# Performance work log

Measured on AMD Instinct MI355X. Metric: run time of the kernel, lower is better.

The kernel has to match this reference:

```python
import jax, jax.numpy as jnp
import numpy as np
from jax import lax

EPS = 1e-5
C, H, W, G = 512, 32, 32, 32


def instance_norm(x):
    # torch InstanceNorm2d: affine=False, biased variance over (H,W)
    mu = x.mean(axis=(2, 3), keepdims=True)
    var = ((x - mu) ** 2).mean(axis=(2, 3), keepdims=True)
    return (x - mu) / jnp.sqrt(var + EPS)


def conv2d(x, w, stride=1, padding=0, groups=1, lhs_dilation=None):
    return lax.conv_general_dilated(
        x, w, (stride, stride), [(padding, padding)] * 2,
        lhs_dilation=lhs_dilation, feature_group_count=groups,
        dimension_numbers=('NCHW', 'OIHW', 'NCHW'))


def leaky_relu(x):
    return jnp.where(x >= 0, x, 0.2 * x)


def unfold(img, k, s):
    # img: (C,H,W) -> (nH*nW, C, k, k); matches torch unfold(1,k,s).unfold(2,k,s)
    c, h, w = img.shape
    nH = (h - k) // s + 1
    nW = (w - k) // s + 1
    rows = []
    for i in range(k):
        cols = [img[:, i:i + s * (nH - 1) + 1:s, j:j + s * (nW - 1) + 1:s] for j in range(k)]
        rows.append(jnp.stack(cols, axis=-1))  # (C,nH,nW,k)
    p = jnp.stack(rows, axis=-2)  # (C,nH,nW,k,k)
    return p.transpose(1, 2, 0, 3, 4).reshape(nH * nW, c, k, k)


def ral(bg, fg, rate=2, ksize=3, scale=10.0):
    # Region Affinity Layer (contextual-attention style), batch = 1
    b, c, h, w = fg.shape
    fh, fw = h // rate, w // rate
    # bilinear downsample by exactly 2 (half-pixel) == 2x2 average pooling
    fg_small = fg.reshape(b, c, fh, rate, fw, rate).mean(axis=(3, 5))
    bk = 2 * rate
    bg_patches = unfold(jnp.pad(bg, ((0, 0), (0, 0), (1, 1), (1, 1)))[0], bk, rate)      # (256,C,4,4)
    fg_patches = unfold(jnp.pad(fg_small, ((0, 0), (0, 0), (1, 1), (1, 1)))[0], ksize, 1)  # (256,C,3,3)
    norm = jnp.sqrt((fg_patches ** 2).sum(axis=(1, 2, 3), keepdims=True))
    fgp_n = fg_patches / jnp.maximum(norm, 1e-4)
    score = conv2d(fg_small, fgp_n, padding=1)        # (1,256,16,16)
    attn = jax.nn.softmax(score * scale, axis=1)
    # conv_transpose2d(attn, bg_patches, stride=rate, padding=1) via lhs dilation
    w_t = jnp.flip(bg_patches, axis=(-2, -1)).transpose(1, 0, 2, 3)  # (C,256,4,4)
    return conv2d(attn, w_t, padding=bk - 2, lhs_dilation=(rate, rate)) / 4.0  # (1,C,32,32)


def forward(x, gus, w_sk3, b_sk3, w_sk5, b_sk5, w_sk7, b_sk7,
            w_fc, b_fc, w_fc0, b_fc0, w_fc1, b_fc1, w_fc2, b_fc2, w_down, w_fuse):
    # ---- SKConv (M=3 branches: k=3/5/7, groups=32) ----
    feas = []
    for wgt, bias, pad in ((w_sk3, b_sk3, 1), (w_sk5, b_sk5, 2), (w_sk7, b_sk7, 3)):
        f = conv2d(x, wgt, padding=pad, groups=G) + bias[None, :, None, None]
        feas.append(jax.nn.relu(instance_norm(f)))
    feas = jnp.stack(feas, axis=1)                # (B,3,C,H,W)
    fea_s = feas.sum(axis=1).mean(axis=(2, 3))    # (B,C) global pool
    fea_z = fea_s @ w_fc.T + b_fc                 # (B,32)
    att = jnp.stack([fea_z @ w_fc0.T + b_fc0,
                     fea_z @ w_fc1.T + b_fc1,
                     fea_z @ w_fc2.T + b_fc2], axis=1)  # (B,3,C)
    att = jax.nn.softmax(att, axis=1)[..., None, None]
    out_32 = (feas * att).sum(axis=1)             # (1,C,32,32)
    out_res = out_32
    out_32 = ral(out_32, out_32)
    b, c, h, w = out_32.shape
    # ---- gaussian-weighted broadcast sum: (P,H,W)x(C,H,W)->(P,C)->raw reshape ----
    gus_out = jnp.einsum('pxy,cxy->pc', gus, out_32[0]).reshape(b, c, h, w)
    # ---- CSA patch correlation ----
    csa2_in = jax.nn.sigmoid(out_32)
    p_fff = unfold(jnp.pad(out_32, ((0, 0), (0, 0), (1, 1), (1, 1)))[0], 3, 1)    # (1024,C,3,3)
    p_f = unfold(jnp.pad(csa2_in, ((0, 0), (0, 0), (1, 1), (1, 1)))[0], 3, 1)     # (1024,C,3,3)
    p_conv = unfold(csa2_in[0], 1, 1)                                             # (1024,C,1,1)
    csa_a = (p_conv * p_f).mean(axis=1)                                           # (1024,3,3)
    csa_a = jax.nn.softmax(csa_a.reshape(h * w, 9), axis=1).reshape(h * w, 1, 3, 3)
    out_csa = (csa_a * p_fff).sum(axis=(-2, -1)).reshape(b, c, h, w)
    # ---- fuse ----
    z = jnp.concatenate([gus_out, out_csa], axis=1)       # (1,1024,32,32)
    z = leaky_relu(instance_norm(conv2d(z, w_down)))
    z = jnp.concatenate([z, out_res], axis=1)             # (1,1024,32,32)
    return leaky_relu(instance_norm(conv2d(z, w_fuse)))   # (1,512,32,32)


def _gaussian_buffer():
    # util.gussin(1.5): gaussian centered at every grid position of a 32x32 map
    v = 1.5
    r = np.arange(32)
    i, k, x, y = np.meshgrid(r, r, r, r, indexing='ij')
    g = np.exp(-((x - i) ** 2 + (y - k) ** 2) / (2 * v * v)) / (2 * np.pi * v * v)
    return jnp.asarray(g.reshape(32 * 32, 32, 32), dtype=jnp.float32)


def setup_inputs():
    key = jax.random.key(0)
    ks = jax.random.split(key, 12)
    s = 0.02
    return {
        'x': jax.random.normal(ks[0], (1, C, H, W), jnp.float32),
        'gus': _gaussian_buffer(),
        'w_sk3': jax.random.normal(ks[1], (C, C // G, 3, 3), jnp.float32) * s,
        'b_sk3': jnp.zeros((C,), jnp.float32),
        'w_sk5': jax.random.normal(ks[2], (C, C // G, 5, 5), jnp.float32) * s,
        'b_sk5': jnp.zeros((C,), jnp.float32),
        'w_sk7': jax.random.normal(ks[3], (C, C // G, 7, 7), jnp.float32) * s,
        'b_sk7': jnp.zeros((C,), jnp.float32),
        'w_fc': jax.random.normal(ks[4], (32, C), jnp.float32) * s,
        'b_fc': jnp.zeros((32,), jnp.float32),
        'w_fc0': jax.random.normal(ks[5], (C, 32), jnp.float32) * s,
        'b_fc0': jnp.zeros((C,), jnp.float32),
        'w_fc1': jax.random.normal(ks[6], (C, 32), jnp.float32) * s,
        'b_fc1': jnp.zeros((C,), jnp.float32),
        'w_fc2': jax.random.normal(ks[7], (C, 32), jnp.float32) * s,
        'b_fc2': jnp.zeros((C,), jnp.float32),
        'w_down': jax.random.normal(ks[8], (512, 1024, 1, 1), jnp.float32) * s,
        'w_fuse': jax.random.normal(ks[9], (512, 1024, 1, 1), jnp.float32) * s,
    }


def reference(x, gus, w_sk3, b_sk3, w_sk5, b_sk5, w_sk7, b_sk7, w_fc, b_fc,
              w_fc0, b_fc0, w_fc1, b_fc1, w_fc2, b_fc2, w_down, w_fuse):
    return forward(x, gus, w_sk3, b_sk3, w_sk5, b_sk5, w_sk7, b_sk7,
                   w_fc, b_fc, w_fc0, b_fc0, w_fc1, b_fc1, w_fc2, b_fc2,
                   w_down, w_fuse)
```

## Files before the change

kernel.cpp:

```cpp
#include <hip/hip_runtime.h>
#include <math.h>

#define EPSN 1e-5f

typedef __attribute__((ext_vector_type(8))) short bf16x8;
typedef __attribute__((ext_vector_type(4))) float f32x4;

__device__ __forceinline__ ushort f2bf(float f) {
  unsigned u = __float_as_uint(f);
  unsigned r = (u + 0x7fff + ((u >> 16) & 1)) >> 16;
  return (ushort)r;
}
__device__ __forceinline__ float bf2f(ushort h) {
  return __uint_as_float(((unsigned)h) << 16);
}

__device__ __forceinline__ void breduce2(float& a, float& b, float* lds) {
#pragma unroll
  for (int o = 32; o > 0; o >>= 1) {
    a += __shfl_down(a, o);
    b += __shfl_down(b, o);
  }
  int lane = threadIdx.x & 63, wid = threadIdx.x >> 6;
  __syncthreads();
  if (lane == 0) { lds[wid] = a; lds[4 + wid] = b; }
  __syncthreads();
  a = lds[0] + lds[1] + lds[2] + lds[3];
  b = lds[4] + lds[5] + lds[6] + lds[7];
}

__device__ __forceinline__ float breduce_sum(float v, float* lds) {
#pragma unroll
  for (int o = 32; o > 0; o >>= 1) v += __shfl_down(v, o);
  int lane = threadIdx.x & 63, wid = threadIdx.x >> 6;
  __syncthreads();
  if (lane == 0) lds[wid] = v;
  __syncthreads();
  return lds[0] + lds[1] + lds[2] + lds[3];
}

__device__ __forceinline__ float breduce_max(float v, float* lds) {
#pragma unroll
  for (int o = 32; o > 0; o >>= 1) v = fmaxf(v, __shfl_down(v, o));
  int lane = threadIdx.x & 63, wid = threadIdx.x >> 6;
  __syncthreads();
  if (lane == 0) lds[wid] = v;
  __syncthreads();
  return fmaxf(fmaxf(lds[0], lds[1]), fmaxf(lds[2], lds[3]));
}

__global__ void pre_kernel(const float* __restrict__ gus,
                           const float* __restrict__ wdown,
                           const float* __restrict__ wfuse,
                           const float* __restrict__ w3,
                           const float* __restrict__ w5,
                           const float* __restrict__ w7,
                           ushort* __restrict__ gus_bf,
                           ushort* __restrict__ wdown_bf,
                           ushort* __restrict__ wfuse_bf,
                           ushort* __restrict__ resd,
                           ushort* __restrict__ Apk_g,
                           ushort* __restrict__ Acomb) {
  int bid = blockIdx.x, tid = threadIdx.x;
  if (bid < 2048) {
    int i = bid * 1024 + tid * 4;
    if (i < 1048576) {
      float4 v = *(const float4*)&gus[i];
      int m = i >> 10, n = i & 1023;
      int y = n >> 5, x = n & 31;
      int idxb = ((y >> 1) << 4) + (x >> 1);
      int py = y & 1;
      ushort2 e0 = {f2bf(v.x), f2bf(v.z)};
      ushort2 e1 = {f2bf(v.y), f2bf(v.w)};
      *(ushort2*)&gus_bf[(size_t)m * 1024 + (py * 2 + 0) * 256 + idxb] = e0;
      *(ushort2*)&gus_bf[(size_t)m * 1024 + (py * 2 + 1) * 256 + idxb] = e1;
    } else {
      const float* src; ushort* dst; int off;
      if (i < 1572864) { src = wdown; dst = wdown_bf; off = i - 1048576; }
      else { src = wfuse; dst = wfuse_bf; off = i - 1572864; }
      float4 v = *(const float4*)&src[off];
      ushort4 o = {f2bf(v.x), f2bf(v.y), f2bf(v.z), f2bf(v.w)};
      *(ushort4*)&dst[off] = o;
    }
  } else if (bid < 2304) {
    int t8 = (bid - 2048) * 256 + tid;
    uint4 z = {0u, 0u, 0u, 0u};
#pragma unroll
    for (int k = 0; k < 4; ++k) *(uint4*)&resd[(size_t)(t8 + k * 65536) * 8] = z;
  } else if (bid < 5056) {
    int i2 = (bid - 2304) * 256 + tid;
    int g = i2 / 22016;
    int r = i2 - g * 22016;
    int p = r >> 9;
    int r5 = r & 511;
    int quad = r5 >> 7, m16 = (r5 >> 3) & 15, j = r & 7;
    int k = quad * 8 + j, tp = k >> 4, ic = k & 15;
    float val = 0.f;
    if (p < 25) {
      int t = 2 * p + tp;
      if (t < 49) val = w7[(size_t)(g * 16 + m16) * 784 + ic * 49 + t];
    } else if (p < 38) {
      int t = 2 * (p - 25) + tp;
      if (t < 25) val = w5[(size_t)(g * 16 + m16) * 400 + ic * 25 + t];
    } else {
      int t = 2 * (p - 38) + tp;
      if (t < 9) val = w3[(size_t)(g * 16 + m16) * 144 + ic * 9 + t];
    }
    Apk_g[i2] = f2bf(val);
  } else {
    int j = (bid - 5056) * 256 + tid;
    uint4 z = {0u, 0u, 0u, 0u};
    ((uint4*)Acomb)[j] = z;
  }
}

__global__ __launch_bounds__(256) void sk_mfma(const float* __restrict__ x,
                                               const ushort* __restrict__ Apk_g,
                                               ushort* __restrict__ feasRawH) {
  __shared__ ushort xg[10 * 38 * 24];
  int bid = blockIdx.x, tid = threadIdx.x;
  int g = bid >> 3, sl = bid & 7, y0 = sl * 4;
  for (int i = tid; i < 4560; i += 256) ((uint*)xg)[i] = 0u;
  __syncthreads();
  for (int i = tid; i < 5120; i += 256) {
    int lr = i >> 9, ic = (i >> 5) & 15, xc = i & 31;
    int y = y0 + lr - 3;
    if ((unsigned)y < 32u)
      xg[(lr * 38 + xc + 3) * 24 + ic] =
          f2bf(x[(size_t)(g * 16 + ic) * 1024 + y * 32 + xc]);
  }
  __syncthreads();
  int wv = tid >> 6, lane = tid & 63, quad = lane >> 4, m16 = lane & 15;
  int qh = (quad & 1) * 8, tp = quad >> 1;
  const ushort* Ag = Apk_g + (size_t)g * 22016;
  f32x4 acc[2][3] = {};
  for (int p = 0; p < 25; ++p) {
    bf16x8 af = *(const bf16x8*)&Ag[(p * 4 + quad) * 128 + m16 * 8];
    int t = 2 * p + tp;
    if (t > 48) t = 48;
    int ky = t / 7, kx = t - ky * 7;
#pragma unroll
    for (int ti = 0; ti < 2; ++ti) {
      int T = wv + ti * 4, tl = T >> 1, x0c = (T & 1) * 16;
      bf16x8 bf = *(const bf16x8*)&xg[((tl + ky) * 38 + x0c + m16 + kx) * 24 + qh];
      acc[ti][2] = __builtin_amdgcn_mfma_f32_16x16x32_bf16(af, bf, acc[ti][2], 0, 0, 0);
    }
  }
  for (int p = 0; p < 13; ++p) {
    bf16x8 af = *(const bf16x8*)&Ag[((p + 25) * 4 + quad) * 128 + m16 * 8];
    int t = 2 * p + tp;
    if (t > 24) t = 24;
    int ky = t / 5, kx = t - ky * 5;
#pragma unroll
    for (int ti = 0; ti < 2; ++ti) {
      int T = wv + ti * 4, tl = T >> 1, x0c = (T & 1) * 16;
      bf16x8 bf =
          *(const bf16x8*)&xg[((tl + ky + 1) * 38 + x0c + m16 + kx + 1) * 24 + qh];
      acc[ti][1] = __builtin_amdgcn_mfma_f32_16x16x32_bf16(af, bf, acc[ti][1], 0, 0, 0);
    }
  }
  for (int p = 0; p < 5; ++p) {
    bf16x8 af = *(const bf16x8*)&Ag[((p + 38) * 4 + quad) * 128 + m16 * 8];
    int t = 2 * p + tp;
    if (t > 8) t = 8;
    int ky = t / 3, kx = t - ky * 3;
#pragma unroll
    for (int ti = 0; ti < 2; ++ti) {
      int T = wv + ti * 4, tl = T >> 1, x0c = (T & 1) * 16;
      bf16x8 bf =
          *(const bf16x8*)&xg[((tl + ky + 2) * 38 + x0c + m16 + kx + 2) * 24 + qh];
      acc[ti][0] = __builtin_amdgcn_mfma_f32_16x16x32_bf16(af, bf, acc[ti][0], 0, 0, 0);
    }
  }
  int cb = g * 16 + quad * 4;
#pragma unroll
  for (int ti = 0; ti < 2; ++ti) {
    int T = wv + ti * 4, tl = T >> 1, x0c = (T & 1) * 16;
    int pos = (y0 + tl) * 32 + x0c + m16;
#pragma unroll
    for (int br = 0; br < 3; ++br)
#pragma unroll
      for (int r = 0; r < 4; ++r)
        feasRawH[(size_t)(br * 512 + cb + r) * 1024 + pos] = f2bf(acc[ti][br][r]);
  }
}

__global__ __launch_bounds__(256) void sk_norm(const ushort* __restrict__ rawH,
                                               ushort* __restrict__ feasH,
                                               float* __restrict__ bmean) {
  __shared__ float red[8];
  int mc = blockIdx.x, tid = threadIdx.x;
  float v[4];
  {
    ushort4 h = *(const ushort4*)&rawH[(size_t)mc * 1024 + tid * 4];
    v[0] = bf2f(h.x); v[1] = bf2f(h.y); v[2] = bf2f(h.z); v[3] = bf2f(h.w);
  }
  float s = 0.f, ss = 0.f;
#pragma unroll
  for (int r = 0; r < 4; ++r) { s += v[r]; ss += v[r] * v[r]; }
  breduce2(s, ss, red);
  float mean = s * (1.f / 1024.f);
  float var = ss * (1.f / 1024.f) - mean * mean;
  float inv = rsqrtf(var + EPSN);
  float rs = 0.f;
  ushort4 o;
#pragma unroll
  for (int r = 0; r < 4; ++r) {
    float t = (v[r] - mean) * inv;
    t = t > 0.f ? t : 0.f;
    ((ushort*)&o)[r] = f2bf(t);
    rs += t;
  }
  *(ushort4*)&feasH[(size_t)mc * 1024 + tid * 4] = o;
  float tot = breduce_sum(rs, red);
  if (tid == 0) bmean[mc] = tot * (1.f / 1024.f);
}

__global__ __launch_bounds__(256) void blend_fc(
    const ushort* __restrict__ feasH, const float* __restrict__ bmean,
    const float* __restrict__ wfc, const float* __restrict__ bfc,
    const float* __restrict__ w0, const float* __restrict__ b0,
    const float* __restrict__ w1, const float* __restrict__ b1,
    const float* __restrict__ w2, const float* __restrict__ b2,
    float* __restrict__ res, ushort* __restrict__ Zt2,
    ushort* __restrict__ resd) {
  __shared__ float sfea[512];
  __shared__ float zpart[8][32];
  __shared__ float zz[32];
  __shared__ float lv[3][32];
  __shared__ float attb[3][32];
  __shared__ float tile[32][33];
  int tid = threadIdx.x;
  int pb = blockIdx.x * 32, cb = blockIdx.y * 32;
  for (int c = tid; c < 512; c += 256)
    sfea[c] = bmean[c] + bmean[512 + c] + bmean[1024 + c];
  __syncthreads();
  {
    int j = tid & 31, seg = tid >> 5;
    float p = 0.f;
    for (int c = seg * 64; c < seg * 64 + 64; ++c) p += sfea[c] * wfc[j * 512 + c];
    zpart[seg][j] = p;
  }
  __syncthreads();
  if (tid < 32) {
    float d = bfc[tid];
#pragma unroll
    for (int s = 0; s < 8; ++s) d += zpart[s][tid];
    zz[tid] = d;
  }
  __syncthreads();
  if (tid < 96) {
    int m = tid >> 5, cl = tid & 31;
    const float* wm = (m == 0) ? w0 : (m == 1) ? w1 : w2;
    const float* bm = (m == 0) ? b0 : (m == 1) ? b1 : b2;
    float l = bm[cb + cl];
#pragma unroll
    for (int j = 0; j < 32; ++j) l += zz[j] * wm[(cb + cl) * 32 + j];
    lv[m][cl] = l;
  }
  __syncthreads();
  if (tid < 32) {
    float l0 = lv[0][tid], l1 = lv[1][tid], l2 = lv[2][tid];
    float mx = fmaxf(l0, fmaxf(l1, l2));
    float e0 = expf(l0 - mx), e1 = expf(l1 - mx), e2 = expf(l2 - mx);
    float inv = 1.f / (e0 + e1 + e2);
    attb[0][tid] = e0 * inv; attb[1][tid] = e1 * inv; attb[2][tid] = e2 * inv;
  }
  __syncthreads();
  int tx = tid & 31, ty = tid >> 5;
  int pos = pb + tx;
  int yy = pos >> 5, xx = pos & 31;
  int ki0 = (yy + 1) & 1, pi0 = (yy + 1 - ki0) >> 1;
  int kj0 = (xx + 1) & 1, pj0 = (xx + 1 - kj0) >> 1;
#pragma unroll
  for (int r = 0; r < 4; ++r) {
    int cl = ty + r * 8;
    int c = cb + cl;
    float v = bf2f(feasH[(size_t)c * 1024 + pos]) * attb[0][cl] +
              bf2f(feasH[(size_t)(512 + c) * 1024 + pos]) * attb[1][cl] +
              bf2f(feasH[(size_t)(1024 + c) * 1024 + pos]) * attb[2][cl];
    res[c * 1024 + pos] = v;
    tile[cl][tx] = v;
    ushort bv16 = f2bf(v);
#pragma unroll
    for (int ai = 0; ai < 2; ++ai) {
      int ki = ki0 + 2 * ai, pi = pi0 - ai;
      if ((unsigned)pi >= 16u) continue;
#pragma unroll
      for (int aj = 0; aj < 2; ++aj) {
        int kj = kj0 + 2 * aj, pj = pj0 - aj;
        if ((unsigned)pj >= 16u) continue;
        resd[((size_t)(ki * 4 + kj) << 17) + (size_t)c * 256 + pi * 16 + pj] = bv16;
      }
    }
  }
  __syncthreads();
#pragma unroll
  for (int r = 0; r < 4; ++r) {
    int pl = ty + r * 8;
    Zt2[(size_t)(pb + pl) * 1024 + 512 + cb + tx] = f2bf(tile[tx][pl]);
  }
}

__global__ __launch_bounds__(256) void gram_part2(const float* __restrict__ res,
                                                  float* __restrict__ Apart) {
  __shared__ float ch[4][324];
  int tid = threadIdx.x;
  int qb = blockIdx.x * 64, pb = blockIdx.y * 64;
  int kc = blockIdx.z;
  int tx = tid & 15, ty = tid >> 4;
  for (int i = tid; i < 4 * 324; i += 256) ((float*)ch)[i] = 0.f;
  int pi = (pb + ty * 4) >> 4, pj = (pb + ty * 4) & 15;
  int qi = (qb + tx * 4) >> 4, qj = (qb + tx * 4) & 15;
  int lane = tid & 63, wv = tid >> 6;
  int sr = lane >> 2, sc = (lane & 3) * 4;
  float acc[4][4] = {};
  for (int c0 = kc * 16; c0 < kc * 16 + 16; c0 += 4) {
    __syncthreads();
    {
      const float* src = res + (size_t)(c0 + wv) * 1024 + (2 * sr) * 32 + 2 * sc;
      float4 r0a = *(const float4*)src;
      float4 r0b = *(const float4*)(src + 4);
      float4 r1a = *(const float4*)(src + 32);
      float4 r1b = *(const float4*)(src + 36);
      float* dst = &ch[wv][(sr + 1) * 18 + sc + 1];
      dst[0] = 0.25f * (r0a.x + r0a.y + r1a.x + r1a.y);
      dst[1] = 0.25f * (r0a.z + r0a.w + r1a.z + r1a.w);
      dst[2] = 0.25f * (r0b.x + r0b.y + r1b.x + r1b.y);
      dst[3] = 0.25f * (r0b.z + r0b.w + r1b.z + r1b.w);
    }
    __syncthreads();
#pragma unroll
    for (int cc = 0; cc < 4; ++cc) {
      float ps[3][6], qs[3][6];
#pragma unroll
      for (int u = 0; u < 3; ++u) {
        const float* pr = &ch[cc][(pi + u) * 18 + pj];
        const float* qr = &ch[cc][(qi + u) * 18 + qj];
#pragma unroll
        for (int t = 0; t < 6; ++t) { ps[u][t] = pr[t]; qs[u][t] = qr[t]; }
      }
#pragma unroll
      for (int u = 0; u < 3; ++u)
#pragma unroll
        for (int v = 0; v < 3; ++v)
#pragma unroll
          for (int i = 0; i < 4; ++i)
#pragma unroll
            for (int j = 0; j < 4; ++j)
              acc[i][j] += ps[u][v + i] * qs[u][v + j];
    }
  }
#pragma unroll
  for (int i = 0; i < 4; ++i) {
    float4 o4 = {acc[i][0], acc[i][1], acc[i][2], acc[i][3]};
    *(float4*)&Apart[(size_t)kc * 65536 + (pb + ty * 4 + i) * 256 + qb + tx * 4] = o4;
  }
}

__global__ __launch_bounds__(256) void attn_soft4(const float* __restrict__ Apart,
                                                  ushort* __restrict__ Acomb) {
  __shared__ float red[8];
  int q = blockIdx.x, t = threadIdx.x;
  float d = 0.f, s = 0.f;
#pragma unroll
  for (int k = 0; k < 32; ++k) {
    d += Apart[(size_t)k * 65536 + t * 257];
    s += Apart[(size_t)k * 65536 + q * 256 + t];
  }
  float invn = 10.f / fmaxf(sqrtf(fmaxf(d, 0.f)), 1e-4f);
  float v = s * invn;
  float mx = breduce_max(v, red);
  float e = expf(v - mx);
  float sm = breduce_sum(e, red);
  ushort val = f2bf(e / sm);
  int qi = q >> 4, qj = q & 15;
#pragma unroll
  for (int ki = 0; ki < 4; ++ki) {
    int y = 2 * qi + ki - 1;
    if ((unsigned)y >= 32u) continue;
#pragma unroll
    for (int kj = 0; kj < 4; ++kj) {
      int x = 2 * qj + kj - 1;
      if ((unsigned)x >= 32u) continue;
      int cls = (y & 1) * 2 + (x & 1);
      int idx = ((y >> 1) << 4) + (x >> 1);
      int seg = ((ki >> 1) << 1) + (kj >> 1);
      Acomb[(size_t)(cls * 256 + idx) * 1024 + seg * 256 + t] = val;
    }
  }
}

__global__ __launch_bounds__(256) void tconv2(const ushort* __restrict__ Acomb,
                                              const ushort* __restrict__ resd,
                                              float* __restrict__ orlt,
                                              float* __restrict__ sigt,
                                              ushort* __restrict__ orlT) {
  __shared__ float tl[64][33];
  int tid = threadIdx.x;
  int wv = tid >> 6, lane = tid & 63, quad = lane >> 4, m16 = lane & 15;
  int nb = blockIdx.x * 32;
  int mb = blockIdx.y * 64;
  int cls = blockIdx.y >> 2;
  int py = cls >> 1, px = cls & 1;
  int row0 = mb + wv * 16 + m16;
  const ushort* Ap = Acomb + (size_t)row0 * 1024 + quad * 8;
  f32x4 ac0 = {0.f, 0.f, 0.f, 0.f}, ac1 = ac0;
#pragma unroll
  for (int sg = 0; sg < 4; ++sg) {
    int ki = 2 * (sg >> 1) + 1 - py;
    int kj = 2 * (sg & 1) + 1 - px;
    const ushort* Bp =
        resd + ((size_t)(ki * 4 + kj) << 17) + (size_t)(nb + m16) * 256 + quad * 8;
    const ushort* As = Ap + sg * 256;
#pragma unroll 2
    for (int k0 = 0; k0 < 256; k0 += 32) {
      bf16x8 af = *(const bf16x8*)(As + k0);
      bf16x8 b0 = *(const bf16x8*)(Bp + k0);
      bf16x8 b1 = *(const bf16x8*)(Bp + 16 * 256 + k0);
      ac0 = __builtin_amdgcn_mfma_f32_16x16x32_bf16(af, b0, ac0, 0, 0, 0);
      ac1 = __builtin_amdgcn_mfma_f32_16x16x32_bf16(af, b1, ac1, 0, 0, 0);
    }
  }
  int rloc0 = wv * 16 + quad * 4;
  f32x4 accs[2] = {ac0, ac1};
#pragma unroll
  for (int nt = 0; nt < 2; ++nt) {
    int c = nb + nt * 16 + m16;
#pragma unroll
    for (int r = 0; r < 4; ++r) {
      int rl = rloc0 + r;
      int idx = (mb + rl) & 255;
      int y = ((idx >> 4) << 1) + py;
      int x = ((idx & 15) << 1) + px;
      int n = y * 32 + x;
      float v = accs[nt][r] * 0.25f;
      orlt[n * 512 + c] = v;
      sigt[n * 512 + c] = 1.f / (1.f + expf(-v));
      tl[rl][nt * 16 + m16] = v;
    }
  }
  __syncthreads();
  int r_l = tid & 63;
#pragma unroll
  for (int k = 0; k < 8; ++k) {
    int c_l = (tid >> 6) + k * 4;
    orlT[(size_t)(nb + c_l) * 1024 + mb + r_l] = f2bf(tl[r_l][c_l]);
  }
}

__global__ __launch_bounds__(256) void gus_csa(
    const ushort* __restrict__ gus_bf, const ushort* __restrict__ orlT,
    const float* __restrict__ sigt, const float* __restrict__ orlt,
    ushort* __restrict__ Zt) {
  __shared__ float red9[4][9];
  __shared__ float a9s[9];
  int tid = threadIdx.x;
  if (blockIdx.x < 128) {
    const int K = 1024;
    int wv = tid >> 6, lane = tid & 63;
    int quad = lane >> 4, m16 = lane & 15;
    int nb = (blockIdx.x & 7) * 64, mb = (blockIdx.x >> 3) * 64;
    const ushort* Ap = gus_bf + (size_t)(mb + wv * 16 + m16) * K + quad * 8;
    const ushort* Bp = orlT + (size_t)(nb + m16) * K + quad * 8;
    f32x4 ac0 = {0.f, 0.f, 0.f, 0.f}, ac1 = ac0, ac2 = ac0, ac3 = ac0;
#pragma unroll 2
    for (int k0 = 0; k0 < K; k0 += 32) {
      bf16x8 af = *(const bf16x8*)(Ap + k0);
      bf16x8 b0 = *(const bf16x8*)(Bp + k0);
      bf16x8 b1 = *(const bf16x8*)(Bp + (size_t)16 * K + k0);
      bf16x8 b2 = *(const bf16x8*)(Bp + (size_t)32 * K + k0);
      bf16x8 b3 = *(const bf16x8*)(Bp + (size_t)48 * K + k0);
      ac0 = __builtin_amdgcn_mfma_f32_16x16x32_bf16(af, b0, ac0, 0, 0, 0);
      ac1 = __builtin_amdgcn_mfma_f32_16x16x32_bf16(af, b1, ac1, 0, 0, 0);
      ac2 = __builtin_amdgcn_mfma_f32_16x16x32_bf16(af, b2, ac2, 0, 0, 0);
      ac3 = __builtin_amdgcn_mfma_f32_16x16x32_bf16(af, b3, ac3, 0, 0, 0);
    }
    int row = mb + wv * 16 + quad * 4;
    f32x4 accs[4] = {ac0, ac1, ac2, ac3};
#pragma unroll
    for (int nt = 0; nt < 4; ++nt) {
      int c = nb + nt * 16 + m16;
#pragma unroll
      for (int r = 0; r < 4; ++r) {
        int p = row + r;
        int pos = ((p & 1) << 9) + c;
        int kk = p >> 1;
        Zt[(size_t)pos * 1024 + kk] = f2bf(accs[nt][r]);
      }
    }
    return;
  }
  int n = blockIdx.x - 128;
  int ny = n >> 5, nx = n & 31;
  int c2 = tid * 2;
  int lane = tid & 63, wid = tid >> 6;
  float2 ctr = *(const float2*)&sigt[n * 512 + c2];
  float part[9];
#pragma unroll
  for (int u = 0; u < 3; ++u) {
    int yy = ny + u - 1;
#pragma unroll
    for (int v = 0; v < 3; ++v) {
      int xx = nx + v - 1;
      float2 nb2 = {0.f, 0.f};
      if ((unsigned)yy < 32u && (unsigned)xx < 32u)
        nb2 = *(const float2*)&sigt[(yy * 32 + xx) * 512 + c2];
      part[u * 3 + v] = ctr.x * nb2.x + ctr.y * nb2.y;
    }
  }
#pragma unroll
  for (int t = 0; t < 9; ++t)
#pragma unroll
    for (int o = 32; o > 0; o >>= 1) part[t] += __shfl_down(part[t], o);
  if (lane == 0)
#pragma unroll
    for (int t = 0; t < 9; ++t) red9[wid][t] = part[t];
  __syncthreads();
  if (tid == 0) {
    float a[9];
#pragma unroll
    for (int t = 0; t < 9; ++t)
      a[t] = (red9[0][t] + red9[1][t] + red9[2][t] + red9[3][t]) * (1.f / 512.f);
    float mx = a[0];
#pragma unroll
    for (int t = 1; t < 9; ++t) mx = fmaxf(mx, a[t]);
    float sum = 0.f;
#pragma unroll
    for (int t = 0; t < 9; ++t) { a[t] = expf(a[t] - mx); sum += a[t]; }
    float inv = 1.f / sum;
#pragma unroll
    for (int t = 0; t < 9; ++t) a9s[t] = a[t] * inv;
  }
  __syncthreads();
  float2 acc = {0.f, 0.f};
#pragma unroll
  for (int u = 0; u < 3; ++u) {
    int yy = ny + u - 1;
#pragma unroll
    for (int v = 0; v < 3; ++v) {
      int xx = nx + v - 1;
      if ((unsigned)yy < 32u && (unsigned)xx < 32u) {
        float w = a9s[u * 3 + v];
        float2 ov = *(const float2*)&orlt[(yy * 32 + xx) * 512 + c2];
        acc.x += w * ov.x;
        acc.y += w * ov.y;
      }
    }
  }
  int kk = 512 + (n >> 1);
  int pos0 = ((n & 1) << 9) + c2;
  Zt[(size_t)pos0 * 1024 + kk] = f2bf(acc.x);
  Zt[(size_t)(pos0 + 1) * 1024 + kk] = f2bf(acc.y);
}

__global__ __launch_bounds__(256) void mfma_gemm_ks(const ushort* __restrict__ A,
                                                    const ushort* __restrict__ Bt,
                                                    float* __restrict__ Cp,
                                                    int N) {
  const int KF = 1024;
  int tid = threadIdx.x;
  int wv = tid >> 6, lane = tid & 63;
  int quad = lane >> 4, m16 = lane & 15;
  int nb = blockIdx.x * 64, mb = blockIdx.y * 64;
  int kh = blockIdx.z;
  const ushort* Ap = A + (size_t)(mb + wv * 16 + m16) * KF + kh * 512 + quad * 8;
  const ushort* Bp = Bt + (size_t)(nb + m16) * KF + kh * 512 + quad * 8;
  f32x4 ac0 = {0.f, 0.f, 0.f, 0.f}, ac1 = ac0, ac2 = ac0, ac3 = ac0;
#pragma unroll 2
  for (int k0 = 0; k0 < 512; k0 += 32) {
    bf16x8 af = *(const bf16x8*)(Ap + k0);
    bf16x8 b0 = *(const bf16x8*)(Bp + k0);
    bf16x8 b1 = *(const bf16x8*)(Bp + (size_t)16 * KF + k0);
    bf16x8 b2 = *(const bf16x8*)(Bp + (size_t)32 * KF + k0);
    bf16x8 b3 = *(const bf16x8*)(Bp + (size_t)48 * KF + k0);
    ac0 = __builtin_amdgcn_mfma_f32_16x16x32_bf16(af, b0, ac0, 0, 0, 0);
    ac1 = __builtin_amdgcn_mfma_f32_16x16x32_bf16(af, b1, ac1, 0, 0, 0);
    ac2 = __builtin_amdgcn_mfma_f32_16x16x32_bf16(af, b2, ac2, 0, 0, 0);
    ac3 = __builtin_amdgcn_mfma_f32_16x16x32_bf16(af, b3, ac3, 0, 0, 0);
  }
  int row = mb + wv * 16 + quad * 4;
  float* C = Cp + (size_t)kh * 524288;
  f32x4 accs[4] = {ac0, ac1, ac2, ac3};
#pragma unroll
  for (int nt = 0; nt < 4; ++nt)
#pragma unroll
    for (int r = 0; r < 4; ++r)
      C[(size_t)(row + r) * N + nb + nt * 16 + m16] = accs[nt][r];
}

__global__ __launch_bounds__(256) void norm_down2(const float* __restrict__ ra,
                                                  ushort* __restrict__ Zt2) {
  __shared__ float red[8];
  int c = blockIdx.x, tid = threadIdx.x;
  float v[4];
  float s = 0.f, ss = 0.f;
#pragma unroll
  for (int r = 0; r < 4; ++r) {
    int i = c * 1024 + tid + r * 256;
    v[r] = ra[i] + ra[524288 + i];
    s += v[r];
    ss += v[r] * v[r];
  }
  breduce2(s, ss, red);
  float mean = s * (1.f / 1024.f);
  float var = ss * (1.f / 1024.f) - mean * mean;
  float inv = rsqrtf(var + EPSN);
#pragma unroll
  for (int r = 0; r < 4; ++r) {
    float t = (v[r] - mean) * inv;
    t = t >= 0.f ? t : 0.2f * t;
    Zt2[(size_t)(tid + r * 256) * 1024 + c] = f2bf(t);
  }
}

__global__ __launch_bounds__(256) void norm_leaky2(const float* __restrict__ ra,
                                                   float* __restrict__ out) {
  __shared__ float red[8];
  int c = blockIdx.x, tid = threadIdx.x;
  float v[4];
  float s = 0.f, ss = 0.f;
#pragma unroll
  for (int r = 0; r < 4; ++r) {
    int i = c * 1024 + tid + r * 256;
    v[r] = ra[i] + ra[524288 + i];
    s += v[r];
    ss += v[r] * v[r];
  }
  breduce2(s, ss, red);
  float mean = s * (1.f / 1024.f);
  float var = ss * (1.f / 1024.f) - mean * mean;
  float inv = rsqrtf(var + EPSN);
#pragma unroll
  for (int r = 0; r < 4; ++r) {
    float t = (v[r] - mean) * inv;
    out[c * 1024 + tid + r * 256] = t >= 0.f ? t : 0.2f * t;
  }
}

extern "C" void kernel_launch(void* const* d_in, const int* in_sizes, int n_in,
                              void* d_out, int out_size, void* d_ws, size_t ws_size,
                              hipStream_t stream) {
  const float* x = (const float*)d_in[0];
  const float* gus = (const float*)d_in[1];
  const float* w3 = (const float*)d_in[2];
  const float* w5 = (const float*)d_in[4];
  const float* w7 = (const float*)d_in[6];
  const float* wfc = (const float*)d_in[8];
  const float* bfc = (const float*)d_in[9];
  const float* w0 = (const float*)d_in[10];
  const float* b0 = (const float*)d_in[11];
  const float* w1 = (const float*)d_in[12];
  const float* b1 = (const float*)d_in[13];
  const float* w2 = (const float*)d_in[14];
  const float* b2 = (const float*)d_in[15];
  const float* wdown = (const float*)d_in[16];
  const float* wfuse = (const float*)d_in[17];

  float* ws = (float*)d_ws;
  ushort* feasH = (ushort*)ws;
  float* rawP = ws + 786432;
  ushort* Acomb = (ushort*)rawP;
  float* bmean = ws + 1835008;
  float* res = bmean + 1536;
  float* Zt2f = res + 524288;
  ushort* Zt2 = (ushort*)Zt2f;
  float* T = Zt2f + 524288;
  ushort* feasRawH = (ushort*)T;
  float* Apart = T;
  ushort* Zt = (ushort*)T;
  float* orlt = T + 2097152;
  float* sigt = orlt + 524288;
  ushort* orlT = (ushort*)(sigt + 524288);
  ushort* gus_bf = (ushort*)(sigt + 819200);
  ushort* wdown_bf = (ushort*)(sigt + 1343488);
  ushort* wfuse_bf = (ushort*)(sigt + 1605632);
  ushort* resd = (ushort*)(sigt + 1867776);
  ushort* Apk_g = (ushort*)(sigt + 2916352);

  pre_kernel<<<5568, 256, 0, stream>>>(gus, wdown, wfuse, w3, w5, w7, gus_bf,
                                       wdown_bf, wfuse_bf, resd, Apk_g, Acomb);
  sk_mfma<<<256, 256, 0, stream>>>(x, Apk_g, feasRawH);
  sk_norm<<<1536, 256, 0, stream>>>(feasRawH, feasH, bmean);
  blend_fc<<<dim3(32, 16), 256, 0, stream>>>(feasH, bmean, wfc, bfc, w0, b0, w1,
                                             b1, w2, b2, res, Zt2, resd);
  gram_part2<<<dim3(4, 4, 32), 256, 0, stream>>>(res, Apart);
  attn_soft4<<<256, 256, 0, stream>>>(Apart, Acomb);
  tconv2<<<dim3(16, 16), 256, 0, stream>>>(Acomb, resd, orlt, sigt, orlT);
  gus_csa<<<1152, 256, 0, stream>>>(gus_bf, orlT, sigt, orlt, Zt);
  mfma_gemm_ks<<<dim3(16, 8, 2), 256, 0, stream>>>(wdown_bf, Zt, rawP, 1024);
  norm_down2<<<512, 256, 0, stream>>>(rawP, Zt2);
  mfma_gemm_ks<<<dim3(16, 8, 2), 256, 0, stream>>>(wfuse_bf, Zt2, rawP, 1024);
  norm_leaky2<<<512, 256, 0, stream>>>(rawP, (float*)d_out);
}
```

Before: 232.8 us.

## Exploit Gram symmetry with upper-triangle tiles, precompute diagonal sums, raise unrolling

The Gram kernel now computes only the 10 upper-triangular 64x64 tile pairs instead of all 16 and mirrors each off-diagonal tile into its transpose. Diagonal entries are accumulated into a small diagsum buffer with atomics, so the softmax kernel no longer performs 32 strided diagonal reads per thread. Separately, the SK convolution loops are fully unrolled and the GEMM inner loops go from unroll 2 to unroll 4. The intent is to cut redundant Gram FLOPs and gather traffic and to improve instruction-level parallelism, at the cost of extra transposed stores, atomics and more register pressure.

New measurement: 217.5 us (median of 3 runs). -6.6%, faster.

```diff
diff --git a/kernel.cpp b/kernel.cpp
--- a/kernel.cpp
+++ b/kernel.cpp
@@ -60,7 +60,8 @@
                            ushort* __restrict__ wfuse_bf,
                            ushort* __restrict__ resd,
                            ushort* __restrict__ Apk_g,
-                           ushort* __restrict__ Acomb) {
+                           ushort* __restrict__ Acomb,
+                           float* __restrict__ diagsum) {
   int bid = blockIdx.x, tid = threadIdx.x;
   if (bid < 2048) {
     int i = bid * 1024 + tid * 4;
@@ -107,10 +108,12 @@
       if (t < 9) val = w3[(size_t)(g * 16 + m16) * 144 + ic * 9 + t];
     }
     Apk_g[i2] = f2bf(val);
-  } else {
+  } else if (bid < 5568) {
     int j = (bid - 5056) * 256 + tid;
     uint4 z = {0u, 0u, 0u, 0u};
     ((uint4*)Acomb)[j] = z;
+  } else {
+    diagsum[tid] = 0.f;
   }
 }
 
@@ -134,6 +137,7 @@
   int qh = (quad & 1) * 8, tp = quad >> 1;
   const ushort* Ag = Apk_g + (size_t)g * 22016;
   f32x4 acc[2][3] = {};
+#pragma unroll
   for (int p = 0; p < 25; ++p) {
     bf16x8 af = *(const bf16x8*)&Ag[(p * 4 + quad) * 128 + m16 * 8];
     int t = 2 * p + tp;
@@ -146,6 +150,7 @@
       acc[ti][2] = __builtin_amdgcn_mfma_f32_16x16x32_bf16(af, bf, acc[ti][2], 0, 0, 0);
     }
   }
+#pragma unroll
   for (int p = 0; p < 13; ++p) {
     bf16x8 af = *(const bf16x8*)&Ag[((p + 25) * 4 + quad) * 128 + m16 * 8];
     int t = 2 * p + tp;
@@ -159,6 +164,7 @@
       acc[ti][1] = __builtin_amdgcn_mfma_f32_16x16x32_bf16(af, bf, acc[ti][1], 0, 0, 0);
     }
   }
+#pragma unroll
   for (int p = 0; p < 5; ++p) {
     bf16x8 af = *(const bf16x8*)&Ag[((p + 38) * 4 + quad) * 128 + m16 * 8];
     int t = 2 * p + tp;
@@ -303,10 +309,14 @@
 }
 
 __global__ __launch_bounds__(256) void gram_part2(const float* __restrict__ res,
-                                                  float* __restrict__ Apart) {
+                                                  float* __restrict__ Apart,
+                                                  float* __restrict__ diagsum) {
   __shared__ float ch[4][324];
+  const int PBT[10] = {0, 0, 0, 0, 1, 1, 1, 2, 2, 3};
+  const int QBT[10] = {0, 1, 2, 3, 1, 2, 3, 2, 3, 3};
   int tid = threadIdx.x;
-  int qb = blockIdx.x * 64, pb = blockIdx.y * 64;
+  int pid = blockIdx.x;
+  int pb = PBT[pid] * 64, qb = QBT[pid] * 64;
   int kc = blockIdx.z;
   int tx = tid & 15, ty = tid >> 4;
   for (int i = tid; i < 4 * 324; i += 256) ((float*)ch)[i] = 0.f;
@@ -356,18 +366,27 @@
     float4 o4 = {acc[i][0], acc[i][1], acc[i][2], acc[i][3]};
     *(float4*)&Apart[(size_t)kc * 65536 + (pb + ty * 4 + i) * 256 + qb + tx * 4] = o4;
   }
+  if (pb != qb) {
+#pragma unroll
+    for (int j = 0; j < 4; ++j) {
+      float4 o4 = {acc[0][j], acc[1][j], acc[2][j], acc[3][j]};
+      *(float4*)&Apart[(size_t)kc * 65536 + (qb + tx * 4 + j) * 256 + pb + ty * 4] = o4;
+    }
+  } else if (tx == ty) {
+#pragma unroll
+    for (int i = 0; i < 4; ++i) atomicAdd(&diagsum[pb + tx * 4 + i], acc[i][i]);
+  }
 }
 
 __global__ __launch_bounds__(256) void attn_soft4(const float* __restrict__ Apart,
+                                                  const float* __restrict__ diagsum,
                                                   ushort* __restrict__ Acomb) {
   __shared__ float red[8];
   int q = blockIdx.x, t = threadIdx.x;
-  float d = 0.f, s = 0.f;
-#pragma unroll
-  for (int k = 0; k < 32; ++k) {
-    d += Apart[(size_t)k * 65536 + t * 257];
-    s += Apart[(size_t)k * 65536 + q * 256 + t];
-  }
+  float d = diagsum[t];
+  float s = 0.f;
+#pragma unroll
+  for (int k = 0; k < 32; ++k) s += Apart[(size_t)k * 65536 + q * 256 + t];
   float invn = 10.f / fmaxf(sqrtf(fmaxf(d, 0.f)), 1e-4f);
   float v = s * invn;
   float mx = breduce_max(v, red);
@@ -413,7 +432,7 @@
     const ushort* Bp =
         resd + ((size_t)(ki * 4 + kj) << 17) + (size_t)(nb + m16) * 256 + quad * 8;
     const ushort* As = Ap + sg * 256;
-#pragma unroll 2
+#pragma unroll 4
     for (int k0 = 0; k0 < 256; k0 += 32) {
       bf16x8 af = *(const bf16x8*)(As + k0);
       bf16x8 b0 = *(const bf16x8*)(Bp + k0);
@@ -464,7 +483,7 @@
     const ushort* Ap = gus_bf + (size_t)(mb + wv * 16 + m16) * K + quad * 8;
     const ushort* Bp = orlT + (size_t)(nb + m16) * K + quad * 8;
     f32x4 ac0 = {0.f, 0.f, 0.f, 0.f}, ac1 = ac0, ac2 = ac0, ac3 = ac0;
-#pragma unroll 2
+#pragma unroll 4
     for (int k0 = 0; k0 < K; k0 += 32) {
       bf16x8 af = *(const bf16x8*)(Ap + k0);
       bf16x8 b0 = *(const bf16x8*)(Bp + k0);
@@ -567,7 +586,7 @@
   const ushort* Ap = A + (size_t)(mb + wv * 16 + m16) * KF + kh * 512 + quad * 8;
   const ushort* Bp = Bt + (size_t)(nb + m16) * KF + kh * 512 + quad * 8;
   f32x4 ac0 = {0.f, 0.f, 0.f, 0.f}, ac1 = ac0, ac2 = ac0, ac3 = ac0;
-#pragma unroll 2
+#pragma unroll 4
   for (int k0 = 0; k0 < 512; k0 += 32) {
     bf16x8 af = *(const bf16x8*)(Ap + k0);
     bf16x8 b0 = *(const bf16x8*)(Bp + k0);
@@ -677,15 +696,17 @@
   ushort* wfuse_bf = (ushort*)(sigt + 1605632);
   ushort* resd = (ushort*)(sigt + 1867776);
   ushort* Apk_g = (ushort*)(sigt + 2916352);
-
-  pre_kernel<<<5568, 256, 0, stream>>>(gus, wdown, wfuse, w3, w5, w7, gus_bf,
-                                       wdown_bf, wfuse_bf, resd, Apk_g, Acomb);
+  float* diagsum = sigt + 3268608;
+
+  pre_kernel<<<5569, 256, 0, stream>>>(gus, wdown, wfuse, w3, w5, w7, gus_bf,
+                                       wdown_bf, wfuse_bf, resd, Apk_g, Acomb,
+                                       diagsum);
   sk_mfma<<<256, 256, 0, stream>>>(x, Apk_g, feasRawH);
   sk_norm<<<1536, 256, 0, stream>>>(feasRawH, feasH, bmean);
   blend_fc<<<dim3(32, 16), 256, 0, stream>>>(feasH, bmean, wfc, bfc, w0, b0, w1,
                                              b1, w2, b2, res, Zt2, resd);
-  gram_part2<<<dim3(4, 4, 32), 256, 0, stream>>>(res, Apart);
-  attn_soft4<<<256, 256, 0, stream>>>(Apart, Acomb);
+  gram_part2<<<dim3(10, 1, 32), 256, 0, stream>>>(res, Apart, diagsum);
+  attn_soft4<<<256, 256, 0, stream>>>(Apart, diagsum, Acomb);
   tconv2<<<dim3(16, 16), 256, 0, stream>>>(Acomb, resd, orlt, sigt, orlT);
   gus_csa<<<1152, 256, 0, stream>>>(gus_bf, orlT, sigt, orlt, Zt);
   mfma_gemm_ks<<<dim3(16, 8, 2), 256, 0, stream>>>(wdown_bf, Zt, rawP, 1024);
```
